# Kernel tuning notes

Measured on AMD Instinct MI355X. Metric: run time of the kernel, lower is better.

## Reference

```python
import jax, jax.numpy as jnp
from jax import lax
import numpy as np


def _conv(x, w, b, stride=1, pad=1):
    # x: [B,C,H,W], w: [O,I,kh,kw]
    y = lax.conv_general_dilated(x, w, (stride, stride), [(pad, pad), (pad, pad)],
                                 dimension_numbers=('NCHW', 'OIHW', 'NCHW'))
    return y + b[None, :, None, None]


def _bn(x, g, b, eps=1e-5):
    # torch BatchNorm2d in training mode: per-channel batch stats, biased variance
    m = jnp.mean(x, axis=(0, 2, 3), keepdims=True)
    v = jnp.var(x, axis=(0, 2, 3), keepdims=True)
    return (x - m) * lax.rsqrt(v + eps) * g[None, :, None, None] + b[None, :, None, None]


def _res_stack(h, w1, b1, w2, b2):
    # one ResidualStack: layers of ReLU->conv3x3->ReLU->conv1x1 with skip, final ReLU
    for i in range(w1.shape[0]):
        t = jnp.maximum(_conv(jnp.maximum(h, 0.0), w1[i], b1[i], 1, 1), 0.0)
        h = h + _conv(t, w2[i], b2[i], 1, 0)
    return jnp.maximum(h, 0.0)


def reference(x, enc_conv0_w, enc_conv0_b, enc_bn0_g, enc_bn0_b, enc_conv1_w, enc_conv1_b,
              enc_bn1_g, enc_bn1_b, enc_conv2_w, enc_conv2_b, enc_res_w1, enc_res_b1,
              enc_res_w2, enc_res_b2, enc_conv3_w, enc_conv3_b, codebook,
              dec_conv0_w, dec_conv0_b, dec_res_w1, dec_res_b1, dec_res_w2, dec_res_b2,
              dec_conv1_w, dec_conv1_b, dec_deconv_w, dec_deconv_b):
    # ---- encoder ----
    h = jnp.maximum(_bn(_conv(x, enc_conv0_w, enc_conv0_b, 2, 1), enc_bn0_g, enc_bn0_b), 0.0)
    h = jnp.maximum(_bn(_conv(h, enc_conv1_w, enc_conv1_b, 1, 1), enc_bn1_g, enc_bn1_b), 0.0)
    h = _conv(h, enc_conv2_w, enc_conv2_b, 1, 1)
    for s in range(enc_res_w1.shape[0]):
        h = _res_stack(h, enc_res_w1[s], enc_res_b1[s], enc_res_w2[s], enc_res_b2[s])
    z = _conv(h, enc_conv3_w, enc_conv3_b, 1, 1)  # [B,D,H,W]
    # ---- vector quantizer ----
    Bz, D, H, W = z.shape
    zf = z.transpose(0, 2, 3, 1).reshape(-1, D)  # [N,D]
    d = (jnp.sum(zf * zf, axis=1, keepdims=True)
         - 2.0 * (zf @ codebook.T)
         + jnp.sum(codebook * codebook, axis=1))  # [N,K]
    idx = jnp.argmin(d, axis=1)
    q = codebook[idx]  # direct gather == one-hot @ codebook
    e_loss = jnp.mean((lax.stop_gradient(q) - zf) ** 2)
    q_loss = jnp.mean((q - lax.stop_gradient(zf)) ** 2)
    vq_loss = q_loss + 0.25 * e_loss
    qst = zf + lax.stop_gradient(q - zf)  # straight-through
    zq = qst.reshape(Bz, H, W, D).transpose(0, 3, 1, 2)
    # ---- decoder ----
    h = _conv(zq, dec_conv0_w, dec_conv0_b, 1, 1)
    for s in range(dec_res_w1.shape[0]):
        h = _res_stack(h, dec_res_w1[s], dec_res_b1[s], dec_res_w2[s], dec_res_b2[s])
    h = jnp.maximum(_conv(h, dec_conv1_w, dec_conv1_b, 1, 1), 0.0)
    # ConvTranspose2d(k=4,s=2,p=1): flip kernel, swap I/O, lhs_dilation=2, pad=k-1-p=2
    wt = jnp.transpose(jnp.flip(dec_deconv_w, (2, 3)), (1, 0, 2, 3))
    xr = lax.conv_general_dilated(h, wt, (1, 1), [(2, 2), (2, 2)], lhs_dilation=(2, 2),
                                  dimension_numbers=('NCHW', 'OIHW', 'NCHW'))
    xr = xr + dec_deconv_b[None, :, None, None]
    recon = jnp.mean((xr - x) ** 2)
    total = recon + vq_loss
    return xr, total, recon


def setup_inputs() -> dict:
    key = jax.random.key(0)
    ks = iter(jax.random.split(key, 64))

    def W(shape):
        fan_in = float(np.prod(shape[-3:]))
        return jax.random.normal(next(ks), shape, jnp.float32) / float(np.sqrt(fan_in))

    def Bv(shape):
        return 0.01 * jax.random.normal(next(ks), shape, jnp.float32)

    inp = {}
    inp['x'] = jax.random.normal(next(ks), (8, 3, 128, 128), jnp.float32)
    inp['enc_conv0_w'] = W((256, 3, 4, 4)); inp['enc_conv0_b'] = Bv((256,))
    inp['enc_bn0_g'] = 1.0 + 0.1 * jax.random.normal(next(ks), (256,), jnp.float32)
    inp['enc_bn0_b'] = Bv((256,))
    inp['enc_conv1_w'] = W((512, 256, 3, 3)); inp['enc_conv1_b'] = Bv((512,))
    inp['enc_bn1_g'] = 1.0 + 0.1 * jax.random.normal(next(ks), (512,), jnp.float32)
    inp['enc_bn1_b'] = Bv((512,))
    inp['enc_conv2_w'] = W((512, 512, 3, 3)); inp['enc_conv2_b'] = Bv((512,))
    inp['enc_res_w1'] = W((4, 4, 128, 512, 3, 3)); inp['enc_res_b1'] = Bv((4, 4, 128))
    inp['enc_res_w2'] = W((4, 4, 512, 128, 1, 1)); inp['enc_res_b2'] = Bv((4, 4, 512))
    inp['enc_conv3_w'] = W((256, 512, 3, 3)); inp['enc_conv3_b'] = Bv((256,))
    inp['codebook'] = jax.random.uniform(next(ks), (1024, 256), jnp.float32, -1.0 / 1024, 1.0 / 1024)
    inp['dec_conv0_w'] = W((512, 256, 3, 3)); inp['dec_conv0_b'] = Bv((512,))
    inp['dec_res_w1'] = W((4, 4, 128, 512, 3, 3)); inp['dec_res_b1'] = Bv((4, 4, 128))
    inp['dec_res_w2'] = W((4, 4, 512, 128, 1, 1)); inp['dec_res_b2'] = Bv((4, 4, 512))
    inp['dec_conv1_w'] = W((256, 512, 3, 3)); inp['dec_conv1_b'] = Bv((256,))
    inp['dec_deconv_w'] = W((256, 3, 4, 4)); inp['dec_deconv_b'] = Bv((3,))
    return inp
```

## Files before the change

kernel.cpp:

```cpp
#include <hip/hip_runtime.h>
#include <cstddef>

#define F_IN_RELU    1
#define F_OUT_RELU   2
#define F_RESIDUAL   4
#define F_COMB       8
#define F_SPLIT      16
#define F_IN_BNORM   32
#define F_STATS      64

typedef __attribute__((ext_vector_type(8))) short short8;
typedef __attribute__((ext_vector_type(4))) short short4v;
typedef __attribute__((ext_vector_type(4))) float floatx4;

__device__ inline float bf2f(short h) {
  union { unsigned int u; float f; } v;
  v.u = ((unsigned int)(unsigned short)h) << 16;
  return v.f;
}
__device__ inline short f2bf(float f) {
  union { float f; unsigned int u; } v; v.f = f;
  unsigned int r = v.u + 0x7fffu + ((v.u >> 16) & 1u);
  return (short)(r >> 16);
}

__global__ void k_init(float* p) {
  for (int i = threadIdx.x; i < 1664; i += 256) p[i] = 0.f;
}

__global__ __launch_bounds__(256) void k_wswz(
    const float* __restrict__ w, short* __restrict__ wq,
    int Cin, int K2, int per_layer)
{
  int idx = blockIdx.x * 256 + threadIdx.x;
  if (idx >= per_layer) return;
  int layer = blockIdx.y;
  w  += (size_t)layer * per_layer;
  wq += (size_t)layer * per_layer;
  int nch = Cin >> 5;
  int j = idx & 7;
  int lane = (idx >> 3) & 63;
  int r = idx >> 9;
  int cich = r % nch; int r2 = r / nch;
  int kk = r2 % K2;   int co_grp = r2 / K2;
  int co = co_grp * 16 + (lane & 15);
  int ci = (cich << 5) + ((lane >> 4) << 3) + j;
  wq[idx] = f2bf(w[((size_t)co * Cin + ci) * K2 + kk]);
}

__global__ __launch_bounds__(256) void k_wswz0m(
    const float* __restrict__ w, short* __restrict__ wq)
{
  int idx = blockIdx.x * 256 + threadIdx.x;
  if (idx >= 16384) return;
  int co = idx >> 6, k = idx & 63;
  float val = (k < 48) ? w[co * 48 + k] : 0.f;
  int cich = k >> 5;
  int lane = (((k >> 3) & 3) << 4) | (co & 15);
  int j = k & 7;
  int cg = co >> 4;
  wq[((size_t)(cg * 2 + cich) * 64 + lane) * 8 + j] = f2bf(val);
}

__global__ __launch_bounds__(256) void k_im2col(
    const float* __restrict__ x, short* __restrict__ out)
{
  int idx = blockIdx.x * 256 + threadIdx.x;
  int k = idx & 63;
  int px = idx >> 6;
  int b = px >> 12;
  int rem = px & 4095;
  int y = rem >> 6, xc = rem & 63;
  int ci = k >> 4, t = k & 15;
  int ky = t >> 2, kx = t & 3;
  float v = 0.f;
  if (ci < 3) {
    int iy = 2 * y - 1 + ky, ix = 2 * xc - 1 + kx;
    if ((unsigned)iy < 128u && (unsigned)ix < 128u)
      v = x[((b * 3 + ci) * 128 + iy) * 128 + ix];
  }
  out[idx] = f2bf(v);
}

__global__ __launch_bounds__(256) void k_wswz_dd(
    const float* __restrict__ w, short* __restrict__ wdt)
{
  int idx = blockIdx.x * 256 + threadIdx.x;
  if (idx >= 12288) return;
  int ci = idx & 255, t = idx >> 8;
  int o = t % 3, kk = t / 3;
  wdt[idx] = f2bf(w[(ci * 3 + o) * 16 + kk]);
}

__global__ __launch_bounds__(256) void k_ccn(
    const float* __restrict__ cb, float* __restrict__ cc)
{
  int code = blockIdx.x * 256 + threadIdx.x;
  const float4* r = (const float4*)(cb + (size_t)code * 256);
  float s = 0.f;
  for (int i = 0; i < 64; ++i) {
    float4 v = r[i];
    s += v.x * v.x + v.y * v.y + v.z * v.z + v.w * v.w;
  }
  cc[code] = s;
}

__global__ __launch_bounds__(512) void k_bnfin(
    const float* __restrict__ sums, const float* __restrict__ g,
    const float* __restrict__ beta, float* __restrict__ ss, int C)
{
  int c = threadIdx.x;
  if (c >= C) return;
  float m = sums[c] * (1.f / 32768.f);
  float var = sums[C + c] * (1.f / 32768.f) - m * m;
  float sc = g[c] * rsqrtf(var + 1e-5f);
  ss[c] = sc;
  ss[C + c] = beta[c] - m * sc;
}

template <int K>
__global__ __launch_bounds__(256) void k_mconv(
    const short* __restrict__ in, short* __restrict__ out,
    short* __restrict__ outf,
    const short* __restrict__ scr2,
    const float* __restrict__ bias_t,
    const float* __restrict__ ss_in, float* __restrict__ sums_out,
    const short* __restrict__ wq, const float* __restrict__ bias,
    int Cin, int c0, int c1, int Cout, int flags)
{
  constexpr int K2 = K * K;
  constexpr int XS = 40;
  constexpr int NR = (K == 3) ? 4 : 1;
  constexpr int NX = (K == 3) ? 66 : 128;
  __shared__ __align__(16) short s_in[NR * NX * XS];
  __shared__ float btl[128];
  __shared__ float ssl[1024];

  int tid = threadIdx.x;
  int lane = tid & 63;
  int wave = tid >> 6;
  int m = lane & 15, quad = lane >> 4;
  int wr = wave >> 1, wc = wave & 1;
  int y2 = blockIdx.y * 2, b = blockIdx.z;
  int coblk = (flags & F_SPLIT) ? 0 : blockIdx.x;
  int nch = Cin >> 5;

  if ((flags & F_COMB) && tid < 128) btl[tid] = bias_t[tid];
  if (flags & F_IN_BNORM) {
    for (int u = tid; u < 2 * Cin; u += 256) ssl[u] = ss_in[u];
  }

  int cc0 = c0, cc1 = c1;
  if (flags & F_SPLIT) {
    int half = nch >> 1;
    cc0 = blockIdx.x * half; cc1 = cc0 + half;
    outf += (size_t)blockIdx.x * 4194304;
  }

  floatx4 acc[4][4];
  #pragma unroll
  for (int f = 0; f < 4; ++f)
    #pragma unroll
    for (int p = 0; p < 4; ++p) acc[f][p] = (floatx4){0.f, 0.f, 0.f, 0.f};

  for (int cich = cc0; cich < cc1; ++cich) {
    __syncthreads();
    if (K == 3) {
      for (int u = tid; u < 4 * 66 * 4; u += 256) {
        int o = u & 3; int t2 = u >> 2;
        int xp = t2 % 66; int row = t2 / 66;
        int gy = y2 - 1 + row, gx = xp - 1;
        int ch = (cich << 5) + (o << 3);
        short8 v = {0, 0, 0, 0, 0, 0, 0, 0};
        if ((unsigned)gy < 64u && (unsigned)gx < 64u)
          v = *(const short8*)&in[((size_t)((b * 64 + gy) * 64 + gx)) * Cin + ch];
        if (flags & F_IN_BNORM) {
          #pragma unroll
          for (int i = 0; i < 8; ++i) {
            float f2 = bf2f(v[i]) * ssl[ch + i] + ssl[Cin + ch + i];
            v[i] = f2bf(f2 > 0.f ? f2 : 0.f);
          }
        } else if (flags & F_IN_RELU) {
          #pragma unroll
          for (int i = 0; i < 8; ++i) if (v[i] < 0) v[i] = 0;
        }
        *(short8*)&s_in[(row * 66 + xp) * XS + (o << 3)] = v;
      }
    } else {
      if (flags & F_COMB) {
        for (int u = tid; u < 512; u += 256) {
          int o = u & 3; int xp = u >> 2;
          int ch = (cich << 5) + (o << 3);
          size_t base = ((size_t)((b * 64 + y2) * 64 + xp)) * 128 + ch;
          float va[8];
          #pragma unroll
          for (int i = 0; i < 8; ++i) va[i] = btl[ch + i];
          #pragma unroll
          for (int q = 0; q < 2; ++q) {
            short8 aq = *(const short8*)&scr2[(size_t)q * 4194304 + base];
            #pragma unroll
            for (int i = 0; i < 8; ++i) va[i] += bf2f(aq[i]);
          }
          short8 v;
          #pragma unroll
          for (int i = 0; i < 8; ++i) v[i] = f2bf(va[i] > 0.f ? va[i] : 0.f);
          *(short8*)&s_in[xp * XS + (o << 3)] = v;
        }
      } else {
        for (int u = tid; u < 512; u += 256) {
          int o = u & 3; int xp = u >> 2;
          short8 v = *(const short8*)&in[((size_t)((b * 64 + y2) * 64 + xp)) * Cin + (cich << 5) + (o << 3)];
          if (flags & F_IN_RELU) {
            #pragma unroll
            for (int i = 0; i < 8; ++i) if (v[i] < 0) v[i] = 0;
          }
          *(short8*)&s_in[xp * XS + (o << 3)] = v;
        }
      }
    }
    __syncthreads();

    #pragma unroll
    for (int kk = 0; kk < K2; ++kk) {
      int ky = (K == 3) ? (kk / 3) : 0;
      int kx = (K == 3) ? (kk - ky * 3) : 0;
      short8 af[4];
      #pragma unroll
      for (int f = 0; f < 4; ++f) {
        int cg = coblk * 8 + wc * 4 + f;
        af[f] = *(const short8*)&wq[(((size_t)(cg * K2 + kk) * nch + cich) * 64 + lane) * 8];
      }
      #pragma unroll
      for (int p = 0; p < 4; ++p) {
        short8 bv;
        if (K == 3)
          bv = *(const short8*)&s_in[((wr + ky) * 66 + p * 16 + m + kx) * XS + (quad << 3)];
        else
          bv = *(const short8*)&s_in[(wr * 64 + p * 16 + m) * XS + (quad << 3)];
        #pragma unroll
        for (int f = 0; f < 4; ++f)
          acc[f][p] = __builtin_amdgcn_mfma_f32_16x16x32_bf16(af[f], bv, acc[f][p], 0, 0, 0);
      }
    }
  }

  int pixrow = (b * 64 + y2 + wr) * 64;

  if (flags & F_SPLIT) {
    #pragma unroll
    for (int f = 0; f < 4; ++f) {
      int co_l = wc * 64 + f * 16 + quad * 4;
      #pragma unroll
      for (int p = 0; p < 4; ++p) {
        int x = p * 16 + m;
        short4v sv;
        #pragma unroll
        for (int r = 0; r < 4; ++r) sv[r] = f2bf(acc[f][p][r]);
        *(short4v*)&outf[(size_t)(pixrow + x) * 128 + co_l] = sv;
      }
    }
    return;
  }

  #pragma unroll
  for (int f = 0; f < 4; ++f) {
    int co4 = coblk * 128 + wc * 64 + f * 16 + quad * 4;
    floatx4 bv4 = *(const floatx4*)&bias[co4];
    float sv1[4] = {0.f, 0.f, 0.f, 0.f};
    float sv2[4] = {0.f, 0.f, 0.f, 0.f};
    #pragma unroll
    for (int p = 0; p < 4; ++p) {
      int x = p * 16 + m;
      size_t oidx = (size_t)(pixrow + x) * Cout + co4;
      float v[4];
      #pragma unroll
      for (int r = 0; r < 4; ++r) v[r] = acc[f][p][r] + bv4[r];
      if (flags & F_RESIDUAL) {
        short4v rr = *(const short4v*)&out[oidx];
        #pragma unroll
        for (int r = 0; r < 4; ++r) v[r] += bf2f(rr[r]);
      }
      if (flags & F_OUT_RELU) {
        #pragma unroll
        for (int r = 0; r < 4; ++r) v[r] = v[r] > 0.f ? v[r] : 0.f;
      }
      if (flags & F_STATS) {
        #pragma unroll
        for (int r = 0; r < 4; ++r) { sv1[r] += v[r]; sv2[r] += v[r] * v[r]; }
      }
      short4v sv;
      #pragma unroll
      for (int r = 0; r < 4; ++r) sv[r] = f2bf(v[r]);
      *(short4v*)&out[oidx] = sv;
    }
    if (flags & F_STATS) {
      #pragma unroll
      for (int r = 0; r < 4; ++r) {
        float a = sv1[r], a2 = sv2[r];
        #pragma unroll
        for (int off = 1; off <= 8; off <<= 1) {
          a += __shfl_xor(a, off);
          a2 += __shfl_xor(a2, off);
        }
        if (m == 0) {
          atomicAdd(&sums_out[co4 + r], a);
          atomicAdd(&sums_out[Cout + co4 + r], a2);
        }
      }
    }
  }
}

__global__ __launch_bounds__(128) void k_vqm(
    const short* __restrict__ z, const short* __restrict__ cbq,
    const float* __restrict__ cb, const float* __restrict__ cc,
    short* __restrict__ zq, float* __restrict__ vq_sum)
{
  __shared__ __align__(16) short zl[64 * 264];
  __shared__ float ccl[1024];
  __shared__ int widx[64];
  __shared__ float red[128];

  int tid = threadIdx.x;
  int lane = tid & 63, wave = tid >> 6;
  int m = lane & 15, quad = lane >> 4;
  size_t px0 = (size_t)blockIdx.x * 64;

  for (int u = tid; u < 64 * 32; u += 128) {
    int px = u >> 5, o = u & 31;
    *(short8*)&zl[px * 264 + o * 8] = *(const short8*)&z[(px0 + px) * 256 + o * 8];
  }
  for (int u = tid; u < 1024; u += 128) ccl[u] = cc[u];
  __syncthreads();

  short8 bf[2][8];
  #pragma unroll
  for (int f = 0; f < 2; ++f) {
    int px = wave * 32 + f * 16 + m;
    #pragma unroll
    for (int kc = 0; kc < 8; ++kc)
      bf[f][kc] = *(const short8*)&zl[px * 264 + kc * 32 + quad * 8];
  }

  float best[2] = {3.4e38f, 3.4e38f};
  int bid[2] = {0, 0};

  for (int cg = 0; cg < 64; ++cg) {
    floatx4 acc0 = (floatx4){0.f, 0.f, 0.f, 0.f};
    floatx4 acc1 = (floatx4){0.f, 0.f, 0.f, 0.f};
    #pragma unroll
    for (int kc = 0; kc < 8; ++kc) {
      short8 af = *(const short8*)&cbq[((size_t)(cg * 8 + kc) * 64 + lane) * 8];
      acc0 = __builtin_amdgcn_mfma_f32_16x16x32_bf16(af, bf[0][kc], acc0, 0, 0, 0);
      acc1 = __builtin_amdgcn_mfma_f32_16x16x32_bf16(af, bf[1][kc], acc1, 0, 0, 0);
    }
    floatx4 c4 = *(const floatx4*)&ccl[cg * 16 + quad * 4];
    #pragma unroll
    for (int r = 0; r < 4; ++r) {
      int code = cg * 16 + quad * 4 + r;
      float s0 = c4[r] - 2.f * acc0[r];
      float s1 = c4[r] - 2.f * acc1[r];
      if (s0 < best[0]) { best[0] = s0; bid[0] = code; }
      if (s1 < best[1]) { best[1] = s1; bid[1] = code; }
    }
  }

  #pragma unroll
  for (int f = 0; f < 2; ++f) {
    float s = best[f]; int i = bid[f];
    #pragma unroll
    for (int off = 16; off <= 32; off <<= 1) {
      float s2 = __shfl_xor(s, off);
      int i2 = __shfl_xor(i, off);
      if (s2 < s || (s2 == s && i2 < i)) { s = s2; i = i2; }
    }
    if (quad == 0) widx[wave * 32 + f * 16 + m] = i;
  }
  __syncthreads();

  float local = 0.f;
  for (int px = 0; px < 64; ++px) {
    int code = widx[px];
    #pragma unroll
    for (int k = 0; k < 2; ++k) {
      int d = tid + k * 128;
      float q = cb[(size_t)code * 256 + d];
      float zv = bf2f(zl[px * 264 + d]);
      float df = q - zv;
      local += df * df;
      zq[(px0 + px) * 256 + d] = f2bf(q);
    }
  }
  red[tid] = local;
  __syncthreads();
  for (int off = 64; off > 0; off >>= 1) {
    if (tid < off) red[tid] += red[tid + off];
    __syncthreads();
  }
  if (tid == 0) atomicAdd(vq_sum, red[0]);
}

__global__ __launch_bounds__(256) void k_deconv(
    const short* __restrict__ h, const short* __restrict__ wdt,
    const float* __restrict__ bias, const float* __restrict__ x,
    float* __restrict__ xr, float* __restrict__ recon_sum)
{
  __shared__ float red[256];
  int idx = blockIdx.x * 256 + threadIdx.x;
  int xc = idx & 127;
  int yc = (idx >> 7) & 127;
  int b = idx >> 14;

  int vy[2], vky[2], nvy = 0;
  int ky0 = (yc + 1) & 1;
  #pragma unroll
  for (int t = 0; t < 2; ++t) {
    int ky = ky0 + 2 * t;
    int iy = (yc + 1 - ky) >> 1;
    if (iy >= 0 && iy < 64) { vky[nvy] = ky; vy[nvy] = iy; ++nvy; }
  }
  int vx[2], vkx[2], nvx = 0;
  int kx0 = (xc + 1) & 1;
  #pragma unroll
  for (int t = 0; t < 2; ++t) {
    int kx = kx0 + 2 * t;
    int ix = (xc + 1 - kx) >> 1;
    if (ix >= 0 && ix < 64) { vkx[nvx] = kx; vx[nvx] = ix; ++nvx; }
  }

  float acc[3] = {bias[0], bias[1], bias[2]};
  for (int ty = 0; ty < nvy; ++ty)
    for (int tx = 0; tx < nvx; ++tx) {
      int kk = vky[ty] * 4 + vkx[tx];
      const short* hp = h + ((size_t)((b * 64 + vy[ty]) * 64 + vx[tx])) * 256;
      const short* wp = wdt + kk * 768;
      for (int c = 0; c < 256; c += 8) {
        short8 hv = *(const short8*)&hp[c];
        short8 w0 = *(const short8*)&wp[c];
        short8 w1 = *(const short8*)&wp[256 + c];
        short8 w2 = *(const short8*)&wp[512 + c];
        #pragma unroll
        for (int i = 0; i < 8; ++i) {
          float hf = bf2f(hv[i]);
          acc[0] += hf * bf2f(w0[i]);
          acc[1] += hf * bf2f(w1[i]);
          acc[2] += hf * bf2f(w2[i]);
        }
      }
    }

  float local = 0.f;
  #pragma unroll
  for (int o = 0; o < 3; ++o) {
    size_t oi = ((size_t)(b * 3 + o) * 128 + yc) * 128 + xc;
    xr[oi] = acc[o];
    float df = acc[o] - x[oi];
    local += df * df;
  }
  red[threadIdx.x] = local;
  __syncthreads();
  for (int off = 128; off > 0; off >>= 1) {
    if (threadIdx.x < off) red[threadIdx.x] += red[threadIdx.x + off];
    __syncthreads();
  }
  if (threadIdx.x == 0) atomicAdd(recon_sum, red[0]);
}

__global__ void k_finalize(const float* __restrict__ a, float* __restrict__ out)
{
  float e = a[0] * (1.f / (32768.f * 256.f));
  float recon = a[1] * (1.f / 393216.f);
  out[393216] = recon + 1.25f * e;
  out[393217] = recon;
}

extern "C" void kernel_launch(void* const* d_in, const int* in_sizes, int n_in,
                              void* d_out, int out_size, void* d_ws, size_t ws_size,
                              hipStream_t stream)
{
  const float* x    = (const float*)d_in[0];
  const float* ec0w = (const float*)d_in[1];
  const float* ec0b = (const float*)d_in[2];
  const float* bn0g = (const float*)d_in[3];
  const float* bn0b = (const float*)d_in[4];
  const float* ec1w = (const float*)d_in[5];
  const float* ec1b = (const float*)d_in[6];
  const float* bn1g = (const float*)d_in[7];
  const float* bn1b = (const float*)d_in[8];
  const float* ec2w = (const float*)d_in[9];
  const float* ec2b = (const float*)d_in[10];
  const float* erw1 = (const float*)d_in[11];
  const float* erb1 = (const float*)d_in[12];
  const float* erw2 = (const float*)d_in[13];
  const float* erb2 = (const float*)d_in[14];
  const float* ec3w = (const float*)d_in[15];
  const float* ec3b = (const float*)d_in[16];
  const float* cb   = (const float*)d_in[17];
  const float* dc0w = (const float*)d_in[18];
  const float* dc0b = (const float*)d_in[19];
  const float* drw1 = (const float*)d_in[20];
  const float* drb1 = (const float*)d_in[21];
  const float* drw2 = (const float*)d_in[22];
  const float* drb2 = (const float*)d_in[23];
  const float* dc1w = (const float*)d_in[24];
  const float* dc1b = (const float*)d_in[25];
  const float* ddw  = (const float*)d_in[26];
  const float* ddb  = (const float*)d_in[27];

  short* wsu = (short*)d_ws;
  short* wq_ec1 = wsu;
  short* wq_ec2 = wsu + 1179648;
  short* wq_ec3 = wsu + 3538944;
  short* wq_dc0 = wsu + 4718592;
  short* wq_dc1 = wsu + 5898240;
  short* wq_er1 = wsu + 7077888;
  short* wq_er2 = wsu + 16515072;
  short* wq_dr1 = wsu + 17563648;
  short* wq_dr2 = wsu + 27000832;
  short* wq_dd  = wsu + 28049408;
  short* cbq    = wsu + 28061696;
  short* wq0    = wsu + 28323840;
  short* im2c   = wsu + 28340224;
  short* bufA   = wsu + 30437376;
  short* bufB   = wsu + 47214592;
  short* bufZ   = wsu + 63991808;
  short* scr    = wsu + 72380416;
  float* stats  = (float*)(wsu + 80769024);
  float* bn0_sums = stats;
  float* bn1_sums = stats + 512;
  float* accums   = stats + 1536;
  float* bn0_ss   = stats + 1664;
  float* bn1_ss   = stats + 2176;
  float* ccn      = stats + 3200;

  k_init<<<1, 256, 0, stream>>>(stats);

  k_wswz0m<<<64, 256, 0, stream>>>(ec0w, wq0);
  k_wswz_dd<<<48, 256, 0, stream>>>(ddw, wq_dd);
  k_ccn<<<4, 256, 0, stream>>>(cb, ccn);
  k_wswz<<<1024, 256, 0, stream>>>(cb, cbq, 256, 1, 262144);
  k_wswz<<<4608, 256, 0, stream>>>(ec1w, wq_ec1, 256, 9, 1179648);
  k_wswz<<<9216, 256, 0, stream>>>(ec2w, wq_ec2, 512, 9, 2359296);
  k_wswz<<<4608, 256, 0, stream>>>(ec3w, wq_ec3, 512, 9, 1179648);
  k_wswz<<<4608, 256, 0, stream>>>(dc0w, wq_dc0, 256, 9, 1179648);
  k_wswz<<<4608, 256, 0, stream>>>(dc1w, wq_dc1, 512, 9, 1179648);
  k_wswz<<<dim3(2304, 16), 256, 0, stream>>>(erw1, wq_er1, 512, 9, 589824);
  k_wswz<<<dim3(256, 16), 256, 0, stream>>>(erw2, wq_er2, 128, 1, 65536);
  k_wswz<<<dim3(2304, 16), 256, 0, stream>>>(drw1, wq_dr1, 512, 9, 589824);
  k_wswz<<<dim3(256, 16), 256, 0, stream>>>(drw2, wq_dr2, 128, 1, 65536);

  k_im2col<<<8192, 256, 0, stream>>>(x, im2c);
  k_mconv<1><<<dim3(2, 32, 8), 256, 0, stream>>>(im2c, bufA, nullptr, nullptr, nullptr,
                                                 nullptr, bn0_sums,
                                                 wq0, ec0b, 64, 0, 2, 256, F_STATS);
  k_bnfin<<<1, 512, 0, stream>>>(bn0_sums, bn0g, bn0b, bn0_ss, 256);
  k_mconv<3><<<dim3(4, 32, 8), 256, 0, stream>>>(bufA, bufB, nullptr, nullptr, nullptr,
                                                 bn0_ss, bn1_sums,
                                                 wq_ec1, ec1b, 256, 0, 8, 512,
                                                 F_IN_BNORM | F_STATS);
  k_bnfin<<<1, 512, 0, stream>>>(bn1_sums, bn1g, bn1b, bn1_ss, 512);
  k_mconv<3><<<dim3(4, 32, 8), 256, 0, stream>>>(bufB, bufA, nullptr, nullptr, nullptr,
                                                 bn1_ss, nullptr,
                                                 wq_ec2, ec2b, 512, 0, 16, 512, F_IN_BNORM);

  for (int l = 0; l < 16; ++l) {
    k_mconv<3><<<dim3(2, 32, 8), 256, 0, stream>>>(bufA, nullptr, scr, nullptr, nullptr,
                                                   nullptr, nullptr,
                                                   wq_er1 + (size_t)l * 589824, nullptr,
                                                   512, 0, 0, 128, F_IN_RELU | F_SPLIT);
    k_mconv<1><<<dim3(4, 32, 8), 256, 0, stream>>>(nullptr, bufA, nullptr, scr,
                                                   erb1 + l * 128, nullptr, nullptr,
                                                   wq_er2 + (size_t)l * 65536, erb2 + l * 512,
                                                   128, 0, 4, 512,
                                                   F_COMB | F_RESIDUAL | (((l & 3) == 3) ? F_OUT_RELU : 0));
  }
  k_mconv<3><<<dim3(2, 32, 8), 256, 0, stream>>>(bufA, bufZ, nullptr, nullptr, nullptr,
                                                 nullptr, nullptr,
                                                 wq_ec3, ec3b, 512, 0, 16, 256, 0);

  k_vqm<<<512, 128, 0, stream>>>(bufZ, cbq, cb, ccn, bufB, accums + 0);

  k_mconv<3><<<dim3(4, 32, 8), 256, 0, stream>>>(bufB, bufA, nullptr, nullptr, nullptr,
                                                 nullptr, nullptr,
                                                 wq_dc0, dc0b, 256, 0, 8, 512, 0);
  for (int l = 0; l < 16; ++l) {
    k_mconv<3><<<dim3(2, 32, 8), 256, 0, stream>>>(bufA, nullptr, scr, nullptr, nullptr,
                                                   nullptr, nullptr,
                                                   wq_dr1 + (size_t)l * 589824, nullptr,
                                                   512, 0, 0, 128, F_IN_RELU | F_SPLIT);
    k_mconv<1><<<dim3(4, 32, 8), 256, 0, stream>>>(nullptr, bufA, nullptr, scr,
                                                   drb1 + l * 128, nullptr, nullptr,
                                                   wq_dr2 + (size_t)l * 65536, drb2 + l * 512,
                                                   128, 0, 4, 512,
                                                   F_COMB | F_RESIDUAL | (((l & 3) == 3) ? F_OUT_RELU : 0));
  }
  k_mconv<3><<<dim3(2, 32, 8), 256, 0, stream>>>(bufA, bufB, nullptr, nullptr, nullptr,
                                                 nullptr, nullptr,
                                                 wq_dc1, dc1b, 512, 0, 16, 256, F_OUT_RELU);

  k_deconv<<<512, 256, 0, stream>>>(bufB, wq_dd, ddb, x, (float*)d_out, accums + 1);
  k_finalize<<<1, 1, 0, stream>>>(accums, (float*)d_out);
}
```

Before: 4.240 ms.

## Fuse residual 3x3 and 1x1 convolutions into one kernel with LDS intermediate

Adds a k_res kernel that computes ReLU -> 3x3 conv -> bias+ReLU into a shared-memory tile, then the 1x1 conv plus bias, residual add and optional ReLU, for each residual layer. It replaces the old pair of launches, a split-K 3x3 conv writing two bf16 partial buffers to scratch and a 1x1 conv that combined them. This removes the scratch round-trip through global memory and halves the launches in the residual stacks. The ping-pong input and output buffers avoid in-place hazards. In exchange, each block now runs the full 512-channel reduction with 512 threads and about 56KB of LDS. The no-longer-needed flag paths are dropped from k_mconv.

New measurement: 3.990 ms. -5.9%, faster.

```diff
diff --git a/kernel.cpp b/kernel.cpp
--- a/kernel.cpp
+++ b/kernel.cpp
@@ -1,11 +1,7 @@
 #include <hip/hip_runtime.h>
 #include <cstddef>
 
-#define F_IN_RELU    1
 #define F_OUT_RELU   2
-#define F_RESIDUAL   4
-#define F_COMB       8
-#define F_SPLIT      16
 #define F_IN_BNORM   32
 #define F_STATS      64
 
@@ -121,19 +117,15 @@
 template <int K>
 __global__ __launch_bounds__(256) void k_mconv(
     const short* __restrict__ in, short* __restrict__ out,
-    short* __restrict__ outf,
-    const short* __restrict__ scr2,
-    const float* __restrict__ bias_t,
     const float* __restrict__ ss_in, float* __restrict__ sums_out,
     const short* __restrict__ wq, const float* __restrict__ bias,
-    int Cin, int c0, int c1, int Cout, int flags)
+    int Cin, int Cout, int flags)
 {
   constexpr int K2 = K * K;
   constexpr int XS = 40;
   constexpr int NR = (K == 3) ? 4 : 1;
   constexpr int NX = (K == 3) ? 66 : 128;
   __shared__ __align__(16) short s_in[NR * NX * XS];
-  __shared__ float btl[128];
   __shared__ float ssl[1024];
 
   int tid = threadIdx.x;
@@ -142,28 +134,20 @@
   int m = lane & 15, quad = lane >> 4;
   int wr = wave >> 1, wc = wave & 1;
   int y2 = blockIdx.y * 2, b = blockIdx.z;
-  int coblk = (flags & F_SPLIT) ? 0 : blockIdx.x;
+  int coblk = blockIdx.x;
   int nch = Cin >> 5;
 
-  if ((flags & F_COMB) && tid < 128) btl[tid] = bias_t[tid];
   if (flags & F_IN_BNORM) {
     for (int u = tid; u < 2 * Cin; u += 256) ssl[u] = ss_in[u];
   }
 
-  int cc0 = c0, cc1 = c1;
-  if (flags & F_SPLIT) {
-    int half = nch >> 1;
-    cc0 = blockIdx.x * half; cc1 = cc0 + half;
-    outf += (size_t)blockIdx.x * 4194304;
-  }
-
   floatx4 acc[4][4];
   #pragma unroll
   for (int f = 0; f < 4; ++f)
     #pragma unroll
     for (int p = 0; p < 4; ++p) acc[f][p] = (floatx4){0.f, 0.f, 0.f, 0.f};
 
-  for (int cich = cc0; cich < cc1; ++cich) {
+  for (int cich = 0; cich < nch; ++cich) {
     __syncthreads();
     if (K == 3) {
       for (int u = tid; u < 4 * 66 * 4; u += 256) {
@@ -180,42 +164,14 @@
             float f2 = bf2f(v[i]) * ssl[ch + i] + ssl[Cin + ch + i];
             v[i] = f2bf(f2 > 0.f ? f2 : 0.f);
           }
-        } else if (flags & F_IN_RELU) {
-          #pragma unroll
-          for (int i = 0; i < 8; ++i) if (v[i] < 0) v[i] = 0;
         }
         *(short8*)&s_in[(row * 66 + xp) * XS + (o << 3)] = v;
       }
     } else {
-      if (flags & F_COMB) {
-        for (int u = tid; u < 512; u += 256) {
-          int o = u & 3; int xp = u >> 2;
-          int ch = (cich << 5) + (o << 3);
-          size_t base = ((size_t)((b * 64 + y2) * 64 + xp)) * 128 + ch;
-          float va[8];
-          #pragma unroll
-          for (int i = 0; i < 8; ++i) va[i] = btl[ch + i];
-          #pragma unroll
-          for (int q = 0; q < 2; ++q) {
-            short8 aq = *(const short8*)&scr2[(size_t)q * 4194304 + base];
-            #pragma unroll
-            for (int i = 0; i < 8; ++i) va[i] += bf2f(aq[i]);
-          }
-          short8 v;
-          #pragma unroll
-          for (int i = 0; i < 8; ++i) v[i] = f2bf(va[i] > 0.f ? va[i] : 0.f);
-          *(short8*)&s_in[xp * XS + (o << 3)] = v;
-        }
-      } else {
-        for (int u = tid; u < 512; u += 256) {
-          int o = u & 3; int xp = u >> 2;
-          short8 v = *(const short8*)&in[((size_t)((b * 64 + y2) * 64 + xp)) * Cin + (cich << 5) + (o << 3)];
-          if (flags & F_IN_RELU) {
-            #pragma unroll
-            for (int i = 0; i < 8; ++i) if (v[i] < 0) v[i] = 0;
-          }
-          *(short8*)&s_in[xp * XS + (o << 3)] = v;
-        }
+      for (int u = tid; u < 512; u += 256) {
+        int o = u & 3; int xp = u >> 2;
+        short8 v = *(const short8*)&in[((size_t)((b * 64 + y2) * 64 + xp)) * Cin + (cich << 5) + (o << 3)];
+        *(short8*)&s_in[xp * XS + (o << 3)] = v;
       }
     }
     __syncthreads();
@@ -246,22 +202,6 @@
 
   int pixrow = (b * 64 + y2 + wr) * 64;
 
-  if (flags & F_SPLIT) {
-    #pragma unroll
-    for (int f = 0; f < 4; ++f) {
-      int co_l = wc * 64 + f * 16 + quad * 4;
-      #pragma unroll
-      for (int p = 0; p < 4; ++p) {
-        int x = p * 16 + m;
-        short4v sv;
-        #pragma unroll
-        for (int r = 0; r < 4; ++r) sv[r] = f2bf(acc[f][p][r]);
-        *(short4v*)&outf[(size_t)(pixrow + x) * 128 + co_l] = sv;
-      }
-    }
-    return;
-  }
-
   #pragma unroll
   for (int f = 0; f < 4; ++f) {
     int co4 = coblk * 128 + wc * 64 + f * 16 + quad * 4;
@@ -275,11 +215,6 @@
       float v[4];
       #pragma unroll
       for (int r = 0; r < 4; ++r) v[r] = acc[f][p][r] + bv4[r];
-      if (flags & F_RESIDUAL) {
-        short4v rr = *(const short4v*)&out[oidx];
-        #pragma unroll
-        for (int r = 0; r < 4; ++r) v[r] += bf2f(rr[r]);
-      }
       if (flags & F_OUT_RELU) {
         #pragma unroll
         for (int r = 0; r < 4; ++r) v[r] = v[r] > 0.f ? v[r] : 0.f;
@@ -307,6 +242,128 @@
           atomicAdd(&sums_out[Cout + co4 + r], a2);
         }
       }
+    }
+  }
+}
+
+__global__ __launch_bounds__(512) void k_res(
+    const short* __restrict__ hin, short* __restrict__ hout,
+    const short* __restrict__ w1q, const float* __restrict__ b1,
+    const short* __restrict__ w2q, const float* __restrict__ b2,
+    int relu_out)
+{
+  constexpr int XS = 40;
+  constexpr int TS = 136;
+  __shared__ __align__(16) short s_in[4 * 66 * XS];
+  __shared__ __align__(16) short t_tile[128 * TS];
+
+  int tid = threadIdx.x;
+  int lane = tid & 63;
+  int wave = tid >> 6;
+  int m = lane & 15, quad = lane >> 4;
+  int wr = wave >> 2;
+  int wq_ = wave & 3;
+  int y2 = blockIdx.x * 2, b = blockIdx.y;
+
+  floatx4 acc[2][4];
+  #pragma unroll
+  for (int f = 0; f < 2; ++f)
+    #pragma unroll
+    for (int p = 0; p < 4; ++p) acc[f][p] = (floatx4){0.f, 0.f, 0.f, 0.f};
+
+  for (int cich = 0; cich < 16; ++cich) {
+    __syncthreads();
+    for (int u = tid; u < 4 * 66 * 4; u += 512) {
+      int o = u & 3; int t2 = u >> 2;
+      int xp = t2 % 66; int row = t2 / 66;
+      int gy = y2 - 1 + row, gx = xp - 1;
+      short8 v = {0, 0, 0, 0, 0, 0, 0, 0};
+      if ((unsigned)gy < 64u && (unsigned)gx < 64u)
+        v = *(const short8*)&hin[((size_t)((b * 64 + gy) * 64 + gx)) * 512 + (cich << 5) + (o << 3)];
+      #pragma unroll
+      for (int i = 0; i < 8; ++i) if (v[i] < 0) v[i] = 0;
+      *(short8*)&s_in[(row * 66 + xp) * XS + (o << 3)] = v;
+    }
+    __syncthreads();
+
+    #pragma unroll
+    for (int kk = 0; kk < 9; ++kk) {
+      int ky = kk / 3, kx = kk - ky * 3;
+      short8 af[2];
+      #pragma unroll
+      for (int f = 0; f < 2; ++f) {
+        int cg = wq_ * 2 + f;
+        af[f] = *(const short8*)&w1q[(((size_t)(cg * 9 + kk) * 16 + cich) * 64 + lane) * 8];
+      }
+      #pragma unroll
+      for (int p = 0; p < 4; ++p) {
+        short8 bv = *(const short8*)&s_in[((wr + ky) * 66 + p * 16 + m + kx) * XS + (quad << 3)];
+        #pragma unroll
+        for (int f = 0; f < 2; ++f)
+          acc[f][p] = __builtin_amdgcn_mfma_f32_16x16x32_bf16(af[f], bv, acc[f][p], 0, 0, 0);
+      }
+    }
+  }
+
+  __syncthreads();
+  #pragma unroll
+  for (int f = 0; f < 2; ++f) {
+    int co4 = wq_ * 32 + f * 16 + quad * 4;
+    floatx4 b4 = *(const floatx4*)&b1[co4];
+    #pragma unroll
+    for (int p = 0; p < 4; ++p) {
+      int pxg = wr * 64 + p * 16 + m;
+      short4v sv;
+      #pragma unroll
+      for (int r = 0; r < 4; ++r) {
+        float v = acc[f][p][r] + b4[r];
+        sv[r] = f2bf(v > 0.f ? v : 0.f);
+      }
+      *(short4v*)&t_tile[pxg * TS + co4] = sv;
+    }
+  }
+  __syncthreads();
+
+  floatx4 acc2[8][4];
+  #pragma unroll
+  for (int f = 0; f < 8; ++f)
+    #pragma unroll
+    for (int p = 0; p < 4; ++p) acc2[f][p] = (floatx4){0.f, 0.f, 0.f, 0.f};
+
+  #pragma unroll
+  for (int cich = 0; cich < 4; ++cich) {
+    short8 bv2[4];
+    #pragma unroll
+    for (int p = 0; p < 4; ++p)
+      bv2[p] = *(const short8*)&t_tile[(wr * 64 + p * 16 + m) * TS + (cich << 5) + (quad << 3)];
+    #pragma unroll
+    for (int f = 0; f < 8; ++f) {
+      int cg2 = wq_ * 8 + f;
+      short8 af2 = *(const short8*)&w2q[(((size_t)cg2 * 4 + cich) * 64 + lane) * 8];
+      #pragma unroll
+      for (int p = 0; p < 4; ++p)
+        acc2[f][p] = __builtin_amdgcn_mfma_f32_16x16x32_bf16(af2, bv2[p], acc2[f][p], 0, 0, 0);
+    }
+  }
+
+  int pixrow = (b * 64 + y2 + wr) * 64;
+  #pragma unroll
+  for (int f = 0; f < 8; ++f) {
+    int co4 = wq_ * 128 + f * 16 + quad * 4;
+    floatx4 b4 = *(const floatx4*)&b2[co4];
+    #pragma unroll
+    for (int p = 0; p < 4; ++p) {
+      int x = p * 16 + m;
+      size_t oidx = (size_t)(pixrow + x) * 512 + co4;
+      short4v rr = *(const short4v*)&hin[oidx];
+      short4v sv;
+      #pragma unroll
+      for (int r = 0; r < 4; ++r) {
+        float v = acc2[f][p][r] + b4[r] + bf2f(rr[r]);
+        if (relu_out) v = v > 0.f ? v : 0.f;
+        sv[r] = f2bf(v);
+      }
+      *(short4v*)&hout[oidx] = sv;
     }
   }
 }
@@ -524,7 +581,6 @@
   short* bufA   = wsu + 30437376;
   short* bufB   = wsu + 47214592;
   short* bufZ   = wsu + 63991808;
-  short* scr    = wsu + 72380416;
   float* stats  = (float*)(wsu + 80769024);
   float* bn0_sums = stats;
   float* bn1_sums = stats + 512;
@@ -550,53 +606,45 @@
   k_wswz<<<dim3(256, 16), 256, 0, stream>>>(drw2, wq_dr2, 128, 1, 65536);
 
   k_im2col<<<8192, 256, 0, stream>>>(x, im2c);
-  k_mconv<1><<<dim3(2, 32, 8), 256, 0, stream>>>(im2c, bufA, nullptr, nullptr, nullptr,
-                                                 nullptr, bn0_sums,
-                                                 wq0, ec0b, 64, 0, 2, 256, F_STATS);
+  k_mconv<1><<<dim3(2, 32, 8), 256, 0, stream>>>(im2c, bufA, nullptr, bn0_sums,
+                                                 wq0, ec0b, 64, 256, F_STATS);
   k_bnfin<<<1, 512, 0, stream>>>(bn0_sums, bn0g, bn0b, bn0_ss, 256);
-  k_mconv<3><<<dim3(4, 32, 8), 256, 0, stream>>>(bufA, bufB, nullptr, nullptr, nullptr,
-                                                 bn0_ss, bn1_sums,
-                                                 wq_ec1, ec1b, 256, 0, 8, 512,
+  k_mconv<3><<<dim3(4, 32, 8), 256, 0, stream>>>(bufA, bufB, bn0_ss, bn1_sums,
+                                                 wq_ec1, ec1b, 256, 512,
                                                  F_IN_BNORM | F_STATS);
   k_bnfin<<<1, 512, 0, stream>>>(bn1_sums, bn1g, bn1b, bn1_ss, 512);
-  k_mconv<3><<<dim3(4, 32, 8), 256, 0, stream>>>(bufB, bufA, nullptr, nullptr, nullptr,
-                                                 bn1_ss, nullptr,
-                                                 wq_ec2, ec2b, 512, 0, 16, 512, F_IN_BNORM);
-
-  for (int l = 0; l < 16; ++l) {
-    k_mconv<3><<<dim3(2, 32, 8), 256, 0, stream>>>(bufA, nullptr, scr, nullptr, nullptr,
-                                                   nullptr, nullptr,
-                                                   wq_er1 + (size_t)l * 589824, nullptr,
-                                                   512, 0, 0, 128, F_IN_RELU | F_SPLIT);
-    k_mconv<1><<<dim3(4, 32, 8), 256, 0, stream>>>(nullptr, bufA, nullptr, scr,
-                                                   erb1 + l * 128, nullptr, nullptr,
-                                                   wq_er2 + (size_t)l * 65536, erb2 + l * 512,
-                                                   128, 0, 4, 512,
-                                                   F_COMB | F_RESIDUAL | (((l & 3) == 3) ? F_OUT_RELU : 0));
-  }
-  k_mconv<3><<<dim3(2, 32, 8), 256, 0, stream>>>(bufA, bufZ, nullptr, nullptr, nullptr,
-                                                 nullptr, nullptr,
-                                                 wq_ec3, ec3b, 512, 0, 16, 256, 0);
+  k_mconv<3><<<dim3(4, 32, 8), 256, 0, stream>>>(bufB, bufA, bn1_ss, nullptr,
+                                                 wq_ec2, ec2b, 512, 512, F_IN_BNORM);
+
+  {
+    short* cur = bufA; short* alt = bufB;
+    for (int l = 0; l < 16; ++l) {
+      k_res<<<dim3(32, 8), 512, 0, stream>>>(cur, alt,
+                                             wq_er1 + (size_t)l * 589824, erb1 + l * 128,
+                                             wq_er2 + (size_t)l * 65536, erb2 + l * 512,
+                                             ((l & 3) == 3) ? 1 : 0);
+      short* tmp = cur; cur = alt; alt = tmp;
+    }
+  }
+  k_mconv<3><<<dim3(2, 32, 8), 256, 0, stream>>>(bufA, bufZ, nullptr, nullptr,
+                                                 wq_ec3, ec3b, 512, 256, 0);
 
   k_vqm<<<512, 128, 0, stream>>>(bufZ, cbq, cb, ccn, bufB, accums + 0);
 
-  k_mconv<3><<<dim3(4, 32, 8), 256, 0, stream>>>(bufB, bufA, nullptr, nullptr, nullptr,
-                                                 nullptr, nullptr,
-                                                 wq_dc0, dc0b, 256, 0, 8, 512, 0);
-  for (int l = 0; l < 16; ++l) {
-    k_mconv<3><<<dim3(2, 32, 8), 256, 0, stream>>>(bufA, nullptr, scr, nullptr, nullptr,
-                                                   nullptr, nullptr,
-                                                   wq_dr1 + (size_t)l * 589824, nullptr,
-                                                   512, 0, 0, 128, F_IN_RELU | F_SPLIT);
-    k_mconv<1><<<dim3(4, 32, 8), 256, 0, stream>>>(nullptr, bufA, nullptr, scr,
-                                                   drb1 + l * 128, nullptr, nullptr,
-                                                   wq_dr2 + (size_t)l * 65536, drb2 + l * 512,
-                                                   128, 0, 4, 512,
-                                                   F_COMB | F_RESIDUAL | (((l & 3) == 3) ? F_OUT_RELU : 0));
-  }
-  k_mconv<3><<<dim3(2, 32, 8), 256, 0, stream>>>(bufA, bufB, nullptr, nullptr, nullptr,
-                                                 nullptr, nullptr,
-                                                 wq_dc1, dc1b, 512, 0, 16, 256, F_OUT_RELU);
+  k_mconv<3><<<dim3(4, 32, 8), 256, 0, stream>>>(bufB, bufA, nullptr, nullptr,
+                                                 wq_dc0, dc0b, 256, 512, 0);
+  {
+    short* cur = bufA; short* alt = bufB;
+    for (int l = 0; l < 16; ++l) {
+      k_res<<<dim3(32, 8), 512, 0, stream>>>(cur, alt,
+                                             wq_dr1 + (size_t)l * 589824, drb1 + l * 128,
+                                             wq_dr2 + (size_t)l * 65536, drb2 + l * 512,
+                                             ((l & 3) == 3) ? 1 : 0);
+      short* tmp = cur; cur = alt; alt = tmp;
+    }
+  }
+  k_mconv<3><<<dim3(2, 32, 8), 256, 0, stream>>>(bufA, bufB, nullptr, nullptr,
+                                                 wq_dc1, dc1b, 512, 256, F_OUT_RELU);
 
   k_deconv<<<512, 256, 0, stream>>>(bufB, wq_dd, ddb, x, (float*)d_out, accums + 1);
   k_finalize<<<1, 1, 0, stream>>>(accums, (float*)d_out);
```
